# Performance work log

Measured on AMD Instinct MI355X. Metric: run time of the kernel, lower is better.

## Reference

```python
import jax, jax.numpy as jnp
import numpy as np

EMBED = 1024
HEADS = 16
DK = EMBED // HEADS


def setup_inputs() -> dict:
    key = jax.random.key(0)
    ks = jax.random.split(key, 6)
    B, S = 2, 2048
    scale = 1.0 / np.sqrt(EMBED)
    x = jax.random.normal(ks[0], (B, S, EMBED), dtype=jnp.float32)
    Wq = jax.random.normal(ks[1], (EMBED, EMBED), dtype=jnp.float32) * scale
    Wk = jax.random.normal(ks[2], (EMBED, EMBED), dtype=jnp.float32) * scale
    Wv = jax.random.normal(ks[3], (EMBED, EMBED), dtype=jnp.float32) * scale
    Wo = jax.random.normal(ks[4], (EMBED, EMBED), dtype=jnp.float32) * scale
    qw = jnp.zeros((HEADS, 1), dtype=jnp.float32)  # quantum_weight, init quantum_scale=0
    return {"x": x, "Wq": Wq, "Wk": Wk, "Wv": Wv, "Wo": Wo, "qw": qw}


def reference(x, Wq, Wk, Wv, Wo, qw):
    B, S, E = x.shape
    # nn.Linear with no bias: y = x @ W.T; split heads -> [B,H,S,Dk]
    def proj(W):
        return (x @ W.T).reshape(B, S, HEADS, DK).transpose(0, 2, 1, 3)
    q, k, v = proj(Wq), proj(Wk), proj(Wv)
    scores = jnp.einsum('bhsd,bhtd->bhst', q, k) / np.sqrt(DK)
    attn = jax.nn.softmax(scores, axis=-1)  # dropout in eval mode: identity
    classical = jnp.einsum('bhst,bhtd->bhsd', attn, v)
    w = jax.nn.sigmoid(qw)[:, :, None]  # [H,1,1] per-head mixing weight
    out = w * jnp.sin(classical) + (1.0 - w) * classical
    out = out.transpose(0, 2, 1, 3).reshape(B, S, E)
    return out @ Wo.T
```

## Files before the change

### kernel.cpp

```cpp
#include <hip/hip_runtime.h>
#include <math.h>

constexpr int Ec  = 1024;
constexpr int Hc  = 16;
constexpr int DKc = 64;
constexpr int Bc  = 2;
constexpr int Sc  = 2048;
constexpr int Mc  = Bc * Sc;

typedef _Float16 half8 __attribute__((ext_vector_type(8)));
typedef _Float16 half4 __attribute__((ext_vector_type(4)));
typedef float    floatx4 __attribute__((ext_vector_type(4)));

#define MFMA16(a, b, c) __builtin_amdgcn_mfma_f32_16x16x32_f16(a, b, c, 0, 0, 0)

__device__ __forceinline__ void async_lds16(const _Float16* g, _Float16* l)
{
    __builtin_amdgcn_global_load_lds(
        (const __attribute__((address_space(1))) unsigned int*)g,
        (__attribute__((address_space(3))) unsigned int*)l, 16, 0, 0);
}

__global__ __launch_bounds__(256)
void convert_to_h(const float4* __restrict__ x,
                  const float4* __restrict__ wq,
                  const float4* __restrict__ wk,
                  const float4* __restrict__ wv,
                  const float4* __restrict__ wo,
                  half4* __restrict__ dst)
{
    const int i = blockIdx.x * 256 + threadIdx.x;
    const float4* src; int off;
    if      (i < 1048576) { src = x;  off = i; }
    else if (i < 1310720) { src = wq; off = i - 1048576; }
    else if (i < 1572864) { src = wk; off = i - 1310720; }
    else if (i < 1835008) { src = wv; off = i - 1572864; }
    else                  { src = wo; off = i - 1835008; }
    const float4 v = src[off];
    half4 o;
    o.x = (_Float16)v.x; o.y = (_Float16)v.y;
    o.z = (_Float16)v.z; o.w = (_Float16)v.w;
    dst[i] = o;
}

__device__ __forceinline__ void mfma_gemm_core(const _Float16* __restrict__ A,
                                               const _Float16* __restrict__ Bw,
                                               int m0, int n0,
                                               _Float16* As, _Float16* Bs,
                                               floatx4 acc[4][4])
{
    const int tid  = threadIdx.x;
    const int wave = tid >> 6, lane = tid & 63;
    const int l16  = lane & 15, quad = lane >> 4;
    const int wrow = (wave >> 1) * 64, wcol = (wave & 1) * 64;

    const int srow = wave * 32 + (lane >> 2);
    const int kseg = (lane & 3) * 8;
    const _Float16* ga = A  + (size_t)(m0 + srow) * Ec + kseg;
    const _Float16* gb = Bw + (size_t)(n0 + srow) * Ec + kseg;
    _Float16* lA = As + wave * 1024;
    _Float16* lB = Bs + wave * 1024;

    for (int kt = 0; kt < Ec; kt += 32) {
        async_lds16(ga,             lA);
        async_lds16(ga + 16 * Ec,   lA + 512);
        async_lds16(gb,             lB);
        async_lds16(gb + 16 * Ec,   lB + 512);
        ga += 32; gb += 32;
        __syncthreads();

        half8 af[4], bf[4];
#pragma unroll
        for (int i = 0; i < 4; ++i)
            af[i] = *(const half8*)&As[(wrow + i * 16 + l16) * 32 + quad * 8];
#pragma unroll
        for (int j = 0; j < 4; ++j)
            bf[j] = *(const half8*)&Bs[(wcol + j * 16 + l16) * 32 + quad * 8];
#pragma unroll
        for (int i = 0; i < 4; ++i)
#pragma unroll
            for (int j = 0; j < 4; ++j)
                acc[i][j] = MFMA16(af[i], bf[j], acc[i][j]);
        __syncthreads();
    }
}

__global__ __launch_bounds__(256)
void gemm_qkv_mfma(const _Float16* __restrict__ xh,
                   const _Float16* __restrict__ wqh,
                   const _Float16* __restrict__ wkh,
                   const _Float16* __restrict__ wvh,
                   _Float16* __restrict__ Qh,
                   _Float16* __restrict__ Kh,
                   _Float16* __restrict__ VTh)
{
    __shared__ __align__(16) _Float16 As[128 * 32];
    __shared__ __align__(16) _Float16 Bs[128 * 32];
    const int z = blockIdx.z;
    const _Float16* W = (z == 0) ? wqh : (z == 1) ? wkh : wvh;
    const int m0 = blockIdx.y * 128, n0 = blockIdx.x * 128;

    floatx4 acc[4][4] = {};
    mfma_gemm_core(xh, W, m0, n0, As, Bs, acc);

    const int tid  = threadIdx.x;
    const int wave = tid >> 6, lane = tid & 63;
    const int l16  = lane & 15, quad = lane >> 4;
    const int wrow = (wave >> 1) * 64, wcol = (wave & 1) * 64;

    if (z == 2) {
#pragma unroll
        for (int i = 0; i < 4; ++i)
#pragma unroll
            for (int j = 0; j < 4; ++j) {
                const int n = n0 + wcol + j * 16 + l16;
                const int h = n >> 6, d = n & 63;
#pragma unroll
                for (int r = 0; r < 4; ++r) {
                    const int m = m0 + wrow + i * 16 + quad * 4 + r;
                    const int b = m >> 11, s = m & (Sc - 1);
                    VTh[((size_t)((b * Hc + h) * DKc + d)) * Sc + s] =
                        (_Float16)acc[i][j][r];
                }
            }
    } else {
        _Float16* out = (z == 0) ? Qh : Kh;
        const float scale = (z == 0) ? 0.125f : 1.0f;
#pragma unroll
        for (int i = 0; i < 4; ++i)
#pragma unroll
            for (int j = 0; j < 4; ++j) {
                const int n = n0 + wcol + j * 16 + l16;
#pragma unroll
                for (int r = 0; r < 4; ++r) {
                    const int m = m0 + wrow + i * 16 + quad * 4 + r;
                    out[(size_t)m * Ec + n] = (_Float16)(acc[i][j][r] * scale);
                }
            }
    }
}

__global__ __launch_bounds__(256)
void gemm_out_mfma(const _Float16* __restrict__ A,
                   const _Float16* __restrict__ W,
                   float* __restrict__ C)
{
    __shared__ __align__(16) _Float16 As[128 * 32];
    __shared__ __align__(16) _Float16 Bs[64 * 32];
    const int m0 = blockIdx.y * 128, n0 = blockIdx.x * 64;

    const int tid  = threadIdx.x;
    const int wave = tid >> 6, lane = tid & 63;
    const int l16  = lane & 15, quad = lane >> 4;
    const int wrow = (wave >> 1) * 64, wcol = (wave & 1) * 32;

    const int kseg = (lane & 3) * 8;
    const _Float16* ga = A + (size_t)(m0 + wave * 32 + (lane >> 2)) * Ec + kseg;
    const _Float16* gb = W + (size_t)(n0 + wave * 16 + (lane >> 2)) * Ec + kseg;
    _Float16* lA = As + wave * 1024;
    _Float16* lB = Bs + wave * 512;

    floatx4 acc[4][2] = {};

    for (int kt = 0; kt < Ec; kt += 32) {
        async_lds16(ga,           lA);
        async_lds16(ga + 16 * Ec, lA + 512);
        async_lds16(gb,           lB);
        ga += 32; gb += 32;
        __syncthreads();

        half8 af[4], bf[2];
#pragma unroll
        for (int i = 0; i < 4; ++i)
            af[i] = *(const half8*)&As[(wrow + i * 16 + l16) * 32 + quad * 8];
#pragma unroll
        for (int j = 0; j < 2; ++j)
            bf[j] = *(const half8*)&Bs[(wcol + j * 16 + l16) * 32 + quad * 8];
#pragma unroll
        for (int i = 0; i < 4; ++i)
#pragma unroll
            for (int j = 0; j < 2; ++j)
                acc[i][j] = MFMA16(af[i], bf[j], acc[i][j]);
        __syncthreads();
    }

#pragma unroll
    for (int i = 0; i < 4; ++i)
#pragma unroll
        for (int j = 0; j < 2; ++j) {
            const int n = n0 + wcol + j * 16 + l16;
#pragma unroll
            for (int r = 0; r < 4; ++r) {
                const int m = m0 + wrow + i * 16 + quad * 4 + r;
                C[(size_t)m * Ec + n] = acc[i][j][r];
            }
        }
}

__global__ __launch_bounds__(256)
void flash_attn(const _Float16* __restrict__ Qh,
                const _Float16* __restrict__ Kh,
                const _Float16* __restrict__ VTh,
                const float* __restrict__ qw,
                _Float16* __restrict__ Mixh)
{
    constexpr int BM = 128, BN = 64, LDH = 72;
    __shared__ _Float16 Kt[BN][LDH];
    __shared__ _Float16 Vt[DKc][LDH];
    __shared__ _Float16 Ps[BM][LDH];

    const int tid  = threadIdx.x;
    const int wave = tid >> 6, lane = tid & 63;
    const int quad = lane >> 4, l16 = lane & 15;
    const int q0 = blockIdx.x * BM;
    const int bh = blockIdx.y;
    const int h  = bh & (Hc - 1), b = bh >> 4;

    half8 aq[2][2];
#pragma unroll
    for (int u = 0; u < 2; ++u) {
        const _Float16* qp = Qh + (size_t)(b * Sc + q0 + wave * 32 + u * 16 + l16) * Ec
                                + h * DKc + quad * 8;
        aq[u][0] = *(const half8*)qp;
        aq[u][1] = *(const half8*)(qp + 32);
    }

    const int srow = tid >> 2;
    const int sseg = (tid & 3) * 16;
    const _Float16* Kg = Kh + (size_t)(b * Sc + srow) * Ec + h * DKc + sseg;
    const _Float16* Vg = VTh + ((size_t)(bh * DKc + srow)) * Sc + sseg;

    half8 kr0 = *(const half8*)Kg, kr1 = *(const half8*)(Kg + 8);
    half8 vr0 = *(const half8*)Vg, vr1 = *(const half8*)(Vg + 8);
    Kg += (size_t)BN * Ec; Vg += BN;
    *(half8*)&Kt[srow][sseg]     = kr0;
    *(half8*)&Kt[srow][sseg + 8] = kr1;

    floatx4 o[2][4] = {};
    float l_run[2] = {0.f, 0.f};

    for (int n = 0; n < Sc / BN; ++n) {
        __syncthreads();
        *(half8*)&Vt[srow][sseg]     = vr0;
        *(half8*)&Vt[srow][sseg + 8] = vr1;
        const bool more = (n + 1 < Sc / BN);
        if (more) {
            kr0 = *(const half8*)Kg; kr1 = *(const half8*)(Kg + 8);
            vr0 = *(const half8*)Vg; vr1 = *(const half8*)(Vg + 8);
            Kg += (size_t)BN * Ec; Vg += BN;
        }

        floatx4 st[2][4];
#pragma unroll
        for (int i = 0; i < 4; ++i) {
            const half8 ak0 = *(const half8*)&Kt[i * 16 + l16][quad * 8];
            const half8 ak1 = *(const half8*)&Kt[i * 16 + l16][32 + quad * 8];
            const floatx4 z = {0.f, 0.f, 0.f, 0.f};
            st[0][i] = MFMA16(ak1, aq[0][1], MFMA16(ak0, aq[0][0], z));
            st[1][i] = MFMA16(ak1, aq[1][1], MFMA16(ak0, aq[1][0], z));
        }

#pragma unroll
        for (int u = 0; u < 2; ++u) {
            const int prow = wave * 32 + u * 16 + l16;
#pragma unroll
            for (int i = 0; i < 4; ++i) {
                const float p0 = __expf(st[u][i][0]);
                const float p1 = __expf(st[u][i][1]);
                const float p2 = __expf(st[u][i][2]);
                const float p3 = __expf(st[u][i][3]);
                l_run[u] += (p0 + p1) + (p2 + p3);
                half4 pk;
                pk.x = (_Float16)p0; pk.y = (_Float16)p1;
                pk.z = (_Float16)p2; pk.w = (_Float16)p3;
                *(half4*)&Ps[prow][i * 16 + quad * 4] = pk;
            }
        }
        __syncthreads();

        half8 ap[2][2];
#pragma unroll
        for (int u = 0; u < 2; ++u) {
            const _Float16* pp = &Ps[wave * 32 + u * 16 + l16][quad * 8];
            ap[u][0] = *(const half8*)pp;
            ap[u][1] = *(const half8*)(pp + 32);
        }
#pragma unroll
        for (int jd = 0; jd < 4; ++jd) {
            const half8 bv0 = *(const half8*)&Vt[jd * 16 + l16][quad * 8];
            const half8 bv1 = *(const half8*)&Vt[jd * 16 + l16][32 + quad * 8];
#pragma unroll
            for (int u = 0; u < 2; ++u) {
                o[u][jd] = MFMA16(ap[u][0], bv0, o[u][jd]);
                o[u][jd] = MFMA16(ap[u][1], bv1, o[u][jd]);
            }
        }

        if (more) {
            *(half8*)&Kt[srow][sseg]     = kr0;
            *(half8*)&Kt[srow][sseg + 8] = kr1;
        }
    }

    const float wmix = 1.f / (1.f + __expf(-qw[h]));
#pragma unroll
    for (int u = 0; u < 2; ++u) {
        l_run[u] += __shfl_xor(l_run[u], 16);
        l_run[u] += __shfl_xor(l_run[u], 32);
    }
#pragma unroll
    for (int u = 0; u < 2; ++u)
#pragma unroll
        for (int r = 0; r < 4; ++r) {
            const float l = __shfl(l_run[u], (lane & 48) | (quad * 4 + r));
            const float inv = 1.f / l;
            const int m = q0 + wave * 32 + u * 16 + quad * 4 + r;
            _Float16* mp = Mixh + (size_t)(b * Sc + m) * Ec + h * DKc;
#pragma unroll
            for (int jd = 0; jd < 4; ++jd) {
                const float v = o[u][jd][r] * inv;
                mp[jd * 16 + l16] = (_Float16)(wmix * __sinf(v) + (1.f - wmix) * v);
            }
        }
}

extern "C" void kernel_launch(void* const* d_in, const int* in_sizes, int n_in,
                              void* d_out, int out_size, void* d_ws, size_t ws_size,
                              hipStream_t stream)
{
    const float* x  = (const float*)d_in[0];
    const float* Wq = (const float*)d_in[1];
    const float* Wk = (const float*)d_in[2];
    const float* Wv = (const float*)d_in[3];
    const float* Wo = (const float*)d_in[4];
    const float* qw = (const float*)d_in[5];
    float* out = (float*)d_out;

    _Float16* hb   = (_Float16*)d_ws;
    _Float16* xh   = hb;
    _Float16* wqh  = hb + (size_t)4 * 1024 * 1024;
    _Float16* wkh  = hb + (size_t)5 * 1024 * 1024;
    _Float16* wvh  = hb + (size_t)6 * 1024 * 1024;
    _Float16* woh  = hb + (size_t)7 * 1024 * 1024;
    _Float16* Qh   = hb + (size_t)8 * 1024 * 1024;
    _Float16* Kh   = hb + (size_t)12 * 1024 * 1024;
    _Float16* VTh  = hb + (size_t)16 * 1024 * 1024;
    _Float16* mixh = hb + (size_t)20 * 1024 * 1024;

    convert_to_h<<<dim3(8192), dim3(256), 0, stream>>>(
        (const float4*)x, (const float4*)Wq, (const float4*)Wk,
        (const float4*)Wv, (const float4*)Wo, (half4*)hb);

    gemm_qkv_mfma<<<dim3(Ec / 128, Mc / 128, 3), dim3(256), 0, stream>>>(
        xh, wqh, wkh, wvh, Qh, Kh, VTh);

    flash_attn<<<dim3(Sc / 128, Bc * Hc), dim3(256), 0, stream>>>(
        Qh, Kh, VTh, qw, mixh);

    gemm_out_mfma<<<dim3(Ec / 64, Mc / 128), dim3(256), 0, stream>>>(
        mixh, woh, out);
}
```

Before: 202.9 us.

## Double flash-attention query tile per block and vectorize V-transpose stores

The flash attention kernel now processes 256 query rows per block (64 per wave) instead of 128. This halves the K/V tile loads and LDS staging per query row and doubles MFMA work per barrier. The cost is half as many blocks (256 total), more registers and launch_bounds set to one block per SM, which may hurt occupancy and latency hiding. Separately, the V-transpose epilogue in the QKV GEMM writes four consecutive sequence elements as one half4 store instead of four scalar stores.

```diff
diff --git a/kernel.cpp b/kernel.cpp
--- a/kernel.cpp
+++ b/kernel.cpp
@@ -113,15 +113,14 @@
         for (int i = 0; i < 4; ++i)
 #pragma unroll
             for (int j = 0; j < 4; ++j) {
-                const int n = n0 + wcol + j * 16 + l16;
-                const int h = n >> 6, d = n & 63;
-#pragma unroll
-                for (int r = 0; r < 4; ++r) {
-                    const int m = m0 + wrow + i * 16 + quad * 4 + r;
-                    const int b = m >> 11, s = m & (Sc - 1);
-                    VTh[((size_t)((b * Hc + h) * DKc + d)) * Sc + s] =
-                        (_Float16)acc[i][j][r];
-                }
+                const int n  = n0 + wcol + j * 16 + l16;
+                const int hh = n >> 6, d = n & 63;
+                const int mb = m0 + wrow + i * 16 + quad * 4;
+                const int bb = mb >> 11, s = mb & (Sc - 1);
+                half4 pk;
+#pragma unroll
+                for (int r = 0; r < 4; ++r) pk[r] = (_Float16)acc[i][j][r];
+                *(half4*)&VTh[((size_t)((bb * Hc + hh) * DKc + d)) * Sc + s] = pk;
             }
     } else {
         _Float16* out = (z == 0) ? Qh : Kh;
@@ -197,14 +196,14 @@
         }
 }
 
-__global__ __launch_bounds__(256)
+__global__ __launch_bounds__(256, 1)
 void flash_attn(const _Float16* __restrict__ Qh,
                 const _Float16* __restrict__ Kh,
                 const _Float16* __restrict__ VTh,
                 const float* __restrict__ qw,
                 _Float16* __restrict__ Mixh)
 {
-    constexpr int BM = 128, BN = 64, LDH = 72;
+    constexpr int BM = 256, BN = 64, LDH = 72;
     __shared__ _Float16 Kt[BN][LDH];
     __shared__ _Float16 Vt[DKc][LDH];
     __shared__ _Float16 Ps[BM][LDH];
@@ -216,10 +215,10 @@
     const int bh = blockIdx.y;
     const int h  = bh & (Hc - 1), b = bh >> 4;
 
-    half8 aq[2][2];
-#pragma unroll
-    for (int u = 0; u < 2; ++u) {
-        const _Float16* qp = Qh + (size_t)(b * Sc + q0 + wave * 32 + u * 16 + l16) * Ec
+    half8 aq[4][2];
+#pragma unroll
+    for (int u = 0; u < 4; ++u) {
+        const _Float16* qp = Qh + (size_t)(b * Sc + q0 + wave * 64 + u * 16 + l16) * Ec
                                 + h * DKc + quad * 8;
         aq[u][0] = *(const half8*)qp;
         aq[u][1] = *(const half8*)(qp + 32);
@@ -236,8 +235,8 @@
     *(half8*)&Kt[srow][sseg]     = kr0;
     *(half8*)&Kt[srow][sseg + 8] = kr1;
 
-    floatx4 o[2][4] = {};
-    float l_run[2] = {0.f, 0.f};
+    floatx4 o[4][4] = {};
+    float l_run[4] = {};
 
     for (int n = 0; n < Sc / BN; ++n) {
         __syncthreads();
@@ -250,25 +249,27 @@
             Kg += (size_t)BN * Ec; Vg += BN;
         }
 
-        floatx4 st[2][4];
+        half8 ak0[4], ak1[4];
 #pragma unroll
         for (int i = 0; i < 4; ++i) {
-            const half8 ak0 = *(const half8*)&Kt[i * 16 + l16][quad * 8];
-            const half8 ak1 = *(const half8*)&Kt[i * 16 + l16][32 + quad * 8];
-            const floatx4 z = {0.f, 0.f, 0.f, 0.f};
-            st[0][i] = MFMA16(ak1, aq[0][1], MFMA16(ak0, aq[0][0], z));
-            st[1][i] = MFMA16(ak1, aq[1][1], MFMA16(ak0, aq[1][0], z));
-        }
-
-#pragma unroll
-        for (int u = 0; u < 2; ++u) {
-            const int prow = wave * 32 + u * 16 + l16;
+            ak0[i] = *(const half8*)&Kt[i * 16 + l16][quad * 8];
+            ak1[i] = *(const half8*)&Kt[i * 16 + l16][32 + quad * 8];
+        }
+#pragma unroll
+        for (int u = 0; u < 4; ++u) {
+            floatx4 st[4];
 #pragma unroll
             for (int i = 0; i < 4; ++i) {
-                const float p0 = __expf(st[u][i][0]);
-                const float p1 = __expf(st[u][i][1]);
-                const float p2 = __expf(st[u][i][2]);
-                const float p3 = __expf(st[u][i][3]);
+                const floatx4 z = {0.f, 0.f, 0.f, 0.f};
+                st[i] = MFMA16(ak1[i], aq[u][1], MFMA16(ak0[i], aq[u][0], z));
+            }
+            const int prow = wave * 64 + u * 16 + l16;
+#pragma unroll
+            for (int i = 0; i < 4; ++i) {
+                const float p0 = __expf(st[i][0]);
+                const float p1 = __expf(st[i][1]);
+                const float p2 = __expf(st[i][2]);
+                const float p3 = __expf(st[i][3]);
                 l_run[u] += (p0 + p1) + (p2 + p3);
                 half4 pk;
                 pk.x = (_Float16)p0; pk.y = (_Float16)p1;
@@ -278,10 +279,10 @@
         }
         __syncthreads();
 
-        half8 ap[2][2];
-#pragma unroll
-        for (int u = 0; u < 2; ++u) {
-            const _Float16* pp = &Ps[wave * 32 + u * 16 + l16][quad * 8];
+        half8 ap[4][2];
+#pragma unroll
+        for (int u = 0; u < 4; ++u) {
+            const _Float16* pp = &Ps[wave * 64 + u * 16 + l16][quad * 8];
             ap[u][0] = *(const half8*)pp;
             ap[u][1] = *(const half8*)(pp + 32);
         }
@@ -290,7 +291,7 @@
             const half8 bv0 = *(const half8*)&Vt[jd * 16 + l16][quad * 8];
             const half8 bv1 = *(const half8*)&Vt[jd * 16 + l16][32 + quad * 8];
 #pragma unroll
-            for (int u = 0; u < 2; ++u) {
+            for (int u = 0; u < 4; ++u) {
                 o[u][jd] = MFMA16(ap[u][0], bv0, o[u][jd]);
                 o[u][jd] = MFMA16(ap[u][1], bv1, o[u][jd]);
             }
@@ -304,17 +305,17 @@
 
     const float wmix = 1.f / (1.f + __expf(-qw[h]));
 #pragma unroll
-    for (int u = 0; u < 2; ++u) {
+    for (int u = 0; u < 4; ++u) {
         l_run[u] += __shfl_xor(l_run[u], 16);
         l_run[u] += __shfl_xor(l_run[u], 32);
     }
 #pragma unroll
-    for (int u = 0; u < 2; ++u)
+    for (int u = 0; u < 4; ++u)
 #pragma unroll
         for (int r = 0; r < 4; ++r) {
             const float l = __shfl(l_run[u], (lane & 48) | (quad * 4 + r));
             const float inv = 1.f / l;
-            const int m = q0 + wave * 32 + u * 16 + quad * 4 + r;
+            const int m = q0 + wave * 64 + u * 16 + quad * 4 + r;
             _Float16* mp = Mixh + (size_t)(b * Sc + m) * Ec + h * DKc;
 #pragma unroll
             for (int jd = 0; jd < 4; ++jd) {
@@ -354,7 +355,7 @@
     gemm_qkv_mfma<<<dim3(Ec / 128, Mc / 128, 3), dim3(256), 0, stream>>>(
         xh, wqh, wkh, wvh, Qh, Kh, VTh);
 
-    flash_attn<<<dim3(Sc / 128, Bc * Hc), dim3(256), 0, stream>>>(
+    flash_attn<<<dim3(Sc / 256, Bc * Hc), dim3(256), 0, stream>>>(
         Qh, Kh, VTh, qw, mixh);
 
     gemm_out_mfma<<<dim3(Ec / 64, Mc / 128), dim3(256), 0, stream>>>(
```

Measured after the change: 194.0 us. 1.05x faster.

## Double-buffer K/V tiles in flash attention and vectorize the transposed V store

Applied to the files above, without the earlier changes.

The attention kernel now keeps two LDS buffers each for the K and V tiles. The next tile is written into the spare buffer at the end of each iteration, which lets the kernel drop the block-wide barrier between the softmax P write and the PV matmul. That barrier is not needed because each wave reads only its own rows of Ps. Separately, the V-projection epilogue packs four consecutive sequence positions into one half4 store instead of four scattered 2-byte stores into the transposed VTh layout. The cost is more LDS per block, which may lower occupancy.

```diff
diff --git a/kernel.cpp b/kernel.cpp
--- a/kernel.cpp
+++ b/kernel.cpp
@@ -113,15 +113,14 @@
         for (int i = 0; i < 4; ++i)
 #pragma unroll
             for (int j = 0; j < 4; ++j) {
-                const int n = n0 + wcol + j * 16 + l16;
-                const int h = n >> 6, d = n & 63;
-#pragma unroll
-                for (int r = 0; r < 4; ++r) {
-                    const int m = m0 + wrow + i * 16 + quad * 4 + r;
-                    const int b = m >> 11, s = m & (Sc - 1);
-                    VTh[((size_t)((b * Hc + h) * DKc + d)) * Sc + s] =
-                        (_Float16)acc[i][j][r];
-                }
+                const int n  = n0 + wcol + j * 16 + l16;
+                const int hh = n >> 6, d = n & 63;
+                const int mb = m0 + wrow + i * 16 + quad * 4;
+                const int bb = mb >> 11, s = mb & (Sc - 1);
+                half4 pk;
+#pragma unroll
+                for (int r = 0; r < 4; ++r) pk[r] = (_Float16)acc[i][j][r];
+                *(half4*)&VTh[((size_t)((bb * Hc + hh) * DKc + d)) * Sc + s] = pk;
             }
     } else {
         _Float16* out = (z == 0) ? Qh : Kh;
@@ -205,8 +204,8 @@
                 _Float16* __restrict__ Mixh)
 {
     constexpr int BM = 128, BN = 64, LDH = 72;
-    __shared__ _Float16 Kt[BN][LDH];
-    __shared__ _Float16 Vt[DKc][LDH];
+    __shared__ _Float16 Kt[2][BN][LDH];
+    __shared__ _Float16 Vt[2][DKc][LDH];
     __shared__ _Float16 Ps[BM][LDH];
 
     const int tid  = threadIdx.x;
@@ -230,19 +229,24 @@
     const _Float16* Kg = Kh + (size_t)(b * Sc + srow) * Ec + h * DKc + sseg;
     const _Float16* Vg = VTh + ((size_t)(bh * DKc + srow)) * Sc + sseg;
 
-    half8 kr0 = *(const half8*)Kg, kr1 = *(const half8*)(Kg + 8);
-    half8 vr0 = *(const half8*)Vg, vr1 = *(const half8*)(Vg + 8);
-    Kg += (size_t)BN * Ec; Vg += BN;
-    *(half8*)&Kt[srow][sseg]     = kr0;
-    *(half8*)&Kt[srow][sseg + 8] = kr1;
+    {
+        half8 k0 = *(const half8*)Kg, k1 = *(const half8*)(Kg + 8);
+        half8 v0 = *(const half8*)Vg, v1 = *(const half8*)(Vg + 8);
+        Kg += (size_t)BN * Ec; Vg += BN;
+        *(half8*)&Kt[0][srow][sseg]     = k0;
+        *(half8*)&Kt[0][srow][sseg + 8] = k1;
+        *(half8*)&Vt[0][srow][sseg]     = v0;
+        *(half8*)&Vt[0][srow][sseg + 8] = v1;
+    }
 
     floatx4 o[2][4] = {};
     float l_run[2] = {0.f, 0.f};
 
     for (int n = 0; n < Sc / BN; ++n) {
-        __syncthreads();
-        *(half8*)&Vt[srow][sseg]     = vr0;
-        *(half8*)&Vt[srow][sseg + 8] = vr1;
+        const int buf = n & 1;
+        __syncthreads();
+
+        half8 kr0, kr1, vr0, vr1;
         const bool more = (n + 1 < Sc / BN);
         if (more) {
             kr0 = *(const half8*)Kg; kr1 = *(const half8*)(Kg + 8);
@@ -253,8 +257,8 @@
         floatx4 st[2][4];
 #pragma unroll
         for (int i = 0; i < 4; ++i) {
-            const half8 ak0 = *(const half8*)&Kt[i * 16 + l16][quad * 8];
-            const half8 ak1 = *(const half8*)&Kt[i * 16 + l16][32 + quad * 8];
+            const half8 ak0 = *(const half8*)&Kt[buf][i * 16 + l16][quad * 8];
+            const half8 ak1 = *(const half8*)&Kt[buf][i * 16 + l16][32 + quad * 8];
             const floatx4 z = {0.f, 0.f, 0.f, 0.f};
             st[0][i] = MFMA16(ak1, aq[0][1], MFMA16(ak0, aq[0][0], z));
             st[1][i] = MFMA16(ak1, aq[1][1], MFMA16(ak0, aq[1][0], z));
@@ -276,7 +280,6 @@
                 *(half4*)&Ps[prow][i * 16 + quad * 4] = pk;
             }
         }
-        __syncthreads();
 
         half8 ap[2][2];
 #pragma unroll
@@ -287,8 +290,8 @@
         }
 #pragma unroll
         for (int jd = 0; jd < 4; ++jd) {
-            const half8 bv0 = *(const half8*)&Vt[jd * 16 + l16][quad * 8];
-            const half8 bv1 = *(const half8*)&Vt[jd * 16 + l16][32 + quad * 8];
+            const half8 bv0 = *(const half8*)&Vt[buf][jd * 16 + l16][quad * 8];
+            const half8 bv1 = *(const half8*)&Vt[buf][jd * 16 + l16][32 + quad * 8];
 #pragma unroll
             for (int u = 0; u < 2; ++u) {
                 o[u][jd] = MFMA16(ap[u][0], bv0, o[u][jd]);
@@ -297,8 +300,10 @@
         }
 
         if (more) {
-            *(half8*)&Kt[srow][sseg]     = kr0;
-            *(half8*)&Kt[srow][sseg + 8] = kr1;
+            *(half8*)&Kt[buf ^ 1][srow][sseg]     = kr0;
+            *(half8*)&Kt[buf ^ 1][srow][sseg + 8] = kr1;
+            *(half8*)&Vt[buf ^ 1][srow][sseg]     = vr0;
+            *(half8*)&Vt[buf ^ 1][srow][sseg + 8] = vr1;
         }
     }
 
```

After: 192.9 us. 1.05x faster.

## Double GEMM K-tile to 64 with XOR-swizzled LDS and vectorized V^T stores

Applied to the files above, without the earlier changes.

Both projection GEMMs now stage 64-wide K tiles instead of 32, halving the number of barrier pairs per K loop and issuing more async global-to-LDS loads per step. The LDS layout uses an XOR swizzle on 16-byte chunks to avoid bank conflicts on the fragment reads. The V-transpose epilogue packs four consecutive sequence positions into one half4 store instead of four scalar stores. LDS usage per block doubles, which may reduce occupancy.

```diff
diff --git a/kernel.cpp b/kernel.cpp
--- a/kernel.cpp
+++ b/kernel.cpp
@@ -43,44 +43,50 @@
     dst[i] = o;
 }
 
-__device__ __forceinline__ void mfma_gemm_core(const _Float16* __restrict__ A,
-                                               const _Float16* __restrict__ Bw,
-                                               int m0, int n0,
-                                               _Float16* As, _Float16* Bs,
-                                               floatx4 acc[4][4])
+__device__ __forceinline__ void mfma_gemm_core64(const _Float16* __restrict__ A,
+                                                 const _Float16* __restrict__ Bw,
+                                                 int m0, int n0,
+                                                 _Float16* As, _Float16* Bs,
+                                                 floatx4 acc[4][4])
 {
     const int tid  = threadIdx.x;
     const int wave = tid >> 6, lane = tid & 63;
     const int l16  = lane & 15, quad = lane >> 4;
     const int wrow = (wave >> 1) * 64, wcol = (wave & 1) * 64;
 
-    const int srow = wave * 32 + (lane >> 2);
-    const int kseg = (lane & 3) * 8;
-    const _Float16* ga = A  + (size_t)(m0 + srow) * Ec + kseg;
-    const _Float16* gb = Bw + (size_t)(n0 + srow) * Ec + kseg;
-    _Float16* lA = As + wave * 1024;
-    _Float16* lB = Bs + wave * 1024;
-
-    for (int kt = 0; kt < Ec; kt += 32) {
-        async_lds16(ga,             lA);
-        async_lds16(ga + 16 * Ec,   lA + 512);
-        async_lds16(gb,             lB);
-        async_lds16(gb + 16 * Ec,   lB + 512);
-        ga += 32; gb += 32;
-        __syncthreads();
-
-        half8 af[4], bf[4];
+    const int srow8  = lane >> 3;
+    const int schunk = (lane & 7) ^ (srow8 & 7);
+    const _Float16* ga = A  + (size_t)(m0 + wave * 32 + srow8) * Ec + schunk * 8;
+    const _Float16* gb = Bw + (size_t)(n0 + wave * 32 + srow8) * Ec + schunk * 8;
+    _Float16* lA = As + (size_t)(wave * 32) * 64;
+    _Float16* lB = Bs + (size_t)(wave * 32) * 64;
+
+    for (int kt = 0; kt < Ec; kt += 64) {
+#pragma unroll
+        for (int c = 0; c < 4; ++c) {
+            async_lds16(ga + (size_t)(c * 8) * Ec + kt, lA + c * 512);
+            async_lds16(gb + (size_t)(c * 8) * Ec + kt, lB + c * 512);
+        }
+        __syncthreads();
+
+        half8 af[4][2], bf[4][2];
+#pragma unroll
+        for (int i = 0; i < 4; ++i) {
+            const int ra = wrow + i * 16 + l16;
+            const int rb = wcol + i * 16 + l16;
+#pragma unroll
+            for (int kc = 0; kc < 2; ++kc) {
+                af[i][kc] = *(const half8*)&As[ra * 64 + (((quad + kc * 4) ^ (ra & 7)) * 8)];
+                bf[i][kc] = *(const half8*)&Bs[rb * 64 + (((quad + kc * 4) ^ (rb & 7)) * 8)];
+            }
+        }
 #pragma unroll
         for (int i = 0; i < 4; ++i)
-            af[i] = *(const half8*)&As[(wrow + i * 16 + l16) * 32 + quad * 8];
-#pragma unroll
-        for (int j = 0; j < 4; ++j)
-            bf[j] = *(const half8*)&Bs[(wcol + j * 16 + l16) * 32 + quad * 8];
-#pragma unroll
-        for (int i = 0; i < 4; ++i)
-#pragma unroll
-            for (int j = 0; j < 4; ++j)
-                acc[i][j] = MFMA16(af[i], bf[j], acc[i][j]);
+#pragma unroll
+            for (int j = 0; j < 4; ++j) {
+                acc[i][j] = MFMA16(af[i][0], bf[j][0], acc[i][j]);
+                acc[i][j] = MFMA16(af[i][1], bf[j][1], acc[i][j]);
+            }
         __syncthreads();
     }
 }
@@ -94,14 +100,14 @@
                    _Float16* __restrict__ Kh,
                    _Float16* __restrict__ VTh)
 {
-    __shared__ __align__(16) _Float16 As[128 * 32];
-    __shared__ __align__(16) _Float16 Bs[128 * 32];
+    __shared__ __align__(16) _Float16 As[128 * 64];
+    __shared__ __align__(16) _Float16 Bs[128 * 64];
     const int z = blockIdx.z;
     const _Float16* W = (z == 0) ? wqh : (z == 1) ? wkh : wvh;
     const int m0 = blockIdx.y * 128, n0 = blockIdx.x * 128;
 
     floatx4 acc[4][4] = {};
-    mfma_gemm_core(xh, W, m0, n0, As, Bs, acc);
+    mfma_gemm_core64(xh, W, m0, n0, As, Bs, acc);
 
     const int tid  = threadIdx.x;
     const int wave = tid >> 6, lane = tid & 63;
@@ -113,15 +119,14 @@
         for (int i = 0; i < 4; ++i)
 #pragma unroll
             for (int j = 0; j < 4; ++j) {
-                const int n = n0 + wcol + j * 16 + l16;
-                const int h = n >> 6, d = n & 63;
-#pragma unroll
-                for (int r = 0; r < 4; ++r) {
-                    const int m = m0 + wrow + i * 16 + quad * 4 + r;
-                    const int b = m >> 11, s = m & (Sc - 1);
-                    VTh[((size_t)((b * Hc + h) * DKc + d)) * Sc + s] =
-                        (_Float16)acc[i][j][r];
-                }
+                const int n  = n0 + wcol + j * 16 + l16;
+                const int hh = n >> 6, d = n & 63;
+                const int mb = m0 + wrow + i * 16 + quad * 4;
+                const int bb = mb >> 11, s = mb & (Sc - 1);
+                half4 pk;
+#pragma unroll
+                for (int r = 0; r < 4; ++r) pk[r] = (_Float16)acc[i][j][r];
+                *(half4*)&VTh[((size_t)((bb * Hc + hh) * DKc + d)) * Sc + s] = pk;
             }
     } else {
         _Float16* out = (z == 0) ? Qh : Kh;
@@ -145,8 +150,8 @@
                    const _Float16* __restrict__ W,
                    float* __restrict__ C)
 {
-    __shared__ __align__(16) _Float16 As[128 * 32];
-    __shared__ __align__(16) _Float16 Bs[64 * 32];
+    __shared__ __align__(16) _Float16 As[128 * 64];
+    __shared__ __align__(16) _Float16 Bs[64 * 64];
     const int m0 = blockIdx.y * 128, n0 = blockIdx.x * 64;
 
     const int tid  = threadIdx.x;
@@ -154,33 +159,46 @@
     const int l16  = lane & 15, quad = lane >> 4;
     const int wrow = (wave >> 1) * 64, wcol = (wave & 1) * 32;
 
-    const int kseg = (lane & 3) * 8;
-    const _Float16* ga = A + (size_t)(m0 + wave * 32 + (lane >> 2)) * Ec + kseg;
-    const _Float16* gb = W + (size_t)(n0 + wave * 16 + (lane >> 2)) * Ec + kseg;
-    _Float16* lA = As + wave * 1024;
-    _Float16* lB = Bs + wave * 512;
+    const int srow8  = lane >> 3;
+    const int schunk = (lane & 7) ^ (srow8 & 7);
+    const _Float16* ga = A + (size_t)(m0 + wave * 32 + srow8) * Ec + schunk * 8;
+    const _Float16* gb = W + (size_t)(n0 + wave * 16 + srow8) * Ec + schunk * 8;
+    _Float16* lA = As + (size_t)(wave * 32) * 64;
+    _Float16* lB = Bs + (size_t)(wave * 16) * 64;
 
     floatx4 acc[4][2] = {};
 
-    for (int kt = 0; kt < Ec; kt += 32) {
-        async_lds16(ga,           lA);
-        async_lds16(ga + 16 * Ec, lA + 512);
-        async_lds16(gb,           lB);
-        ga += 32; gb += 32;
-        __syncthreads();
-
-        half8 af[4], bf[2];
+    for (int kt = 0; kt < Ec; kt += 64) {
+#pragma unroll
+        for (int c = 0; c < 4; ++c)
+            async_lds16(ga + (size_t)(c * 8) * Ec + kt, lA + c * 512);
+#pragma unroll
+        for (int c = 0; c < 2; ++c)
+            async_lds16(gb + (size_t)(c * 8) * Ec + kt, lB + c * 512);
+        __syncthreads();
+
+        half8 af[4][2], bf[2][2];
+#pragma unroll
+        for (int i = 0; i < 4; ++i) {
+            const int ra = wrow + i * 16 + l16;
+#pragma unroll
+            for (int kc = 0; kc < 2; ++kc)
+                af[i][kc] = *(const half8*)&As[ra * 64 + (((quad + kc * 4) ^ (ra & 7)) * 8)];
+        }
+#pragma unroll
+        for (int j = 0; j < 2; ++j) {
+            const int rb = wcol + j * 16 + l16;
+#pragma unroll
+            for (int kc = 0; kc < 2; ++kc)
+                bf[j][kc] = *(const half8*)&Bs[rb * 64 + (((quad + kc * 4) ^ (rb & 7)) * 8)];
+        }
 #pragma unroll
         for (int i = 0; i < 4; ++i)
-            af[i] = *(const half8*)&As[(wrow + i * 16 + l16) * 32 + quad * 8];
-#pragma unroll
-        for (int j = 0; j < 2; ++j)
-            bf[j] = *(const half8*)&Bs[(wcol + j * 16 + l16) * 32 + quad * 8];
-#pragma unroll
-        for (int i = 0; i < 4; ++i)
-#pragma unroll
-            for (int j = 0; j < 2; ++j)
-                acc[i][j] = MFMA16(af[i], bf[j], acc[i][j]);
+#pragma unroll
+            for (int j = 0; j < 2; ++j) {
+                acc[i][j] = MFMA16(af[i][0], bf[j][0], acc[i][j]);
+                acc[i][j] = MFMA16(af[i][1], bf[j][1], acc[i][j]);
+            }
         __syncthreads();
     }
 
```

Result: faster. 191.8 us (-5.5%).
